# Kernel optimization log

Measured on AMD Instinct MI355X. Metric: run time of the kernel, lower is better.

## Reference

```python
import jax, jax.numpy as jnp
import numpy as np

N_NODES = 50000


def _sage_conv(x, src, dst, W_l, b_l, W_r):
    # mean aggregation of source-node features at destination nodes
    msg_sum = jax.ops.segment_sum(x[src], dst, num_segments=N_NODES)  # [N, d_in]
    deg = jax.ops.segment_sum(jnp.ones((src.shape[0],), x.dtype), dst,
                              num_segments=N_NODES)  # [N]
    mean = msg_sum / jnp.maximum(deg, 1.0)[:, None]
    # SAGEConv: lin_l(aggr) + lin_r(x); lin_l has bias, lin_r does not
    return mean @ W_l + b_l + x @ W_r


def setup_inputs() -> dict:
    key = jax.random.key(0)
    ks = jax.random.split(key, 8)
    d_in, d_hid, d_out = 128, 128, 64
    E = 800000
    s = lambda k, shp: jax.random.normal(k, shp, dtype=jnp.float32) * (1.0 / np.sqrt(shp[0]))
    return {
        "x": jax.random.normal(ks[0], (N_NODES, d_in), dtype=jnp.float32),
        "edge_index": jax.random.randint(ks[1], (2, E), 0, N_NODES, dtype=jnp.int64
                                         if jax.config.jax_enable_x64 else jnp.int32),
        "W_l1": s(ks[2], (d_in, d_hid)),
        "b_l1": jnp.zeros((d_hid,), jnp.float32),
        "W_r1": s(ks[3], (d_in, d_hid)),
        "W_l2": s(ks[4], (d_hid, d_out)),
        "b_l2": jnp.zeros((d_out,), jnp.float32),
        "W_r2": s(ks[5], (d_hid, d_out)),
    }


def reference(x, edge_index, W_l1, b_l1, W_r1, W_l2, b_l2, W_r2):
    src, dst = edge_index[0], edge_index[1]
    h = _sage_conv(x, src, dst, W_l1, b_l1, W_r1)
    h = jax.nn.relu(h)  # dropout is identity in eval mode
    h = _sage_conv(h, src, dst, W_l2, b_l2, W_r2)
    return h
```

## Files before the change

kernel.cpp:

```cpp
#include <hip/hip_runtime.h>
#include <hip/hip_bf16.h>

#define N_NODES 50000
#define M_TILES 3125
#define NBUCKET 196
#define CHUNK_A 3125
#define PASSB_CAP 12288
#define CONV_BLOCKS 6250

typedef __attribute__((ext_vector_type(8))) __bf16 bf16x8;
typedef __attribute__((ext_vector_type(4))) float f32x4;

#define OFF_OFF   0
#define EBUF_OFF  400384
#define GCUR_OFF  2000384
#define GBASE_OFF 2001408
#define CCNT_OFF  2002432
#define INV_OFF   3800576
#define XBF_OFF   4000768
#define AGG_OFF   16800768
#define HBF_OFF   29600768
#define PBF_OFF   42400768
#define WP1_OFF   48800768
#define WP2_OFF   48866304

__device__ __forceinline__ unsigned bfbits(float f) {
    unsigned u = __float_as_uint(f);
    return (u + 0x7fffu + ((u >> 16) & 1u)) & 0xffff0000u;
}
__device__ __forceinline__ unsigned short bf16r(float f) {
    return (unsigned short)(bfbits(f) >> 16);
}
__device__ __forceinline__ float blo(unsigned u) { return __uint_as_float(u << 16); }
__device__ __forceinline__ float bhi(unsigned u) { return __uint_as_float(u & 0xffff0000u); }

__global__ __launch_bounds__(256) void prep_kernel(const float4* __restrict__ x4,
                                                   uint2* __restrict__ xbf,
                                                   int* __restrict__ ccnt,
                                                   const float* __restrict__ Wl1,
                                                   const float* __restrict__ Wr1,
                                                   const float* __restrict__ Wl2,
                                                   const float* __restrict__ Wr2,
                                                   unsigned short* __restrict__ Wp1,
                                                   unsigned short* __restrict__ Wp2) {
    int bid = blockIdx.x;
    int t = threadIdx.x;
    if (bid < CONV_BLOCKS) {
        if (bid == 0 && t < NBUCKET) ccnt[t] = 0;
        int i = bid * 256 + t;
        float4 v = x4[i];
        uint2 o;
        o.x = (bfbits(v.x) >> 16) | bfbits(v.y);
        o.y = (bfbits(v.z) >> 16) | bfbits(v.w);
        xbf[i] = o;
    } else if (bid < CONV_BLOCKS + 128) {
        int idx = (bid - CONV_BLOCKS) * 256 + t;
        int k = idx >> 7, n = idx & 127;
        float v = (k < 128) ? Wl1[k * 128 + n] : Wr1[(k - 128) * 128 + n];
        Wp1[((k >> 5) << 12) + (n << 5) + (((k >> 3) & 3) << 3) + (k & 7)] = bf16r(v);
    } else {
        int idx = (bid - CONV_BLOCKS - 128) * 256 + t;
        int k = idx >> 7, n = idx & 127;
        float v = (n < 64) ? Wl2[k * 64 + n] : Wr2[k * 64 + (n - 64)];
        Wp2[((k >> 5) << 12) + (n << 5) + (((k >> 3) & 3) << 3) + (k & 7)] = bf16r(v);
    }
}

__global__ __launch_bounds__(256) void histC_kernel(const int* __restrict__ dst,
                                                    int* __restrict__ ccnt, int E) {
    __shared__ int lh[256];
    int t = threadIdx.x;
    lh[t] = 0;
    __syncthreads();
    int e0 = blockIdx.x * CHUNK_A;
    int e1 = min(e0 + CHUNK_A, E);
    for (int e = e0 + t; e < e1; e += 256) atomicAdd(&lh[dst[e] >> 8], 1);
    __syncthreads();
    if (lh[t]) atomicAdd(&ccnt[t], lh[t]);
}

__global__ __launch_bounds__(256) void scanG_kernel(const int* __restrict__ ccnt,
                                                    int* __restrict__ gbase,
                                                    int* __restrict__ gcur,
                                                    int* __restrict__ off, int E) {
    __shared__ int sm[256];
    int t = threadIdx.x;
    int v = (t < NBUCKET) ? ccnt[t] : 0;
    sm[t] = v;
    __syncthreads();
    for (int d = 1; d < 256; d <<= 1) {
        int u = (t >= d) ? sm[t - d] : 0;
        __syncthreads();
        sm[t] += u;
        __syncthreads();
    }
    int excl = sm[t] - v;
    if (t < NBUCKET) {
        gbase[t] = excl;
        gcur[t] = excl;
    }
    if (t == 0) {
        gbase[NBUCKET] = E;
        off[N_NODES] = E;
    }
}

__global__ __launch_bounds__(256) void passA_kernel(const int* __restrict__ src,
                                                    const int* __restrict__ dst,
                                                    int* __restrict__ gcur,
                                                    unsigned* __restrict__ pairs, int E) {
    __shared__ int bh[256];
    __shared__ int lcur[256];
    __shared__ int gb[256];
    __shared__ int sc[256];
    __shared__ unsigned lbuf[3328];
    int t = threadIdx.x;
    int e0 = blockIdx.x * CHUNK_A;
    int e1 = min(e0 + CHUNK_A, E);
    bh[t] = 0;
    lcur[t] = 0;
    __syncthreads();
    for (int e = e0 + t; e < e1; e += 256) atomicAdd(&bh[dst[e] >> 8], 1);
    __syncthreads();
    int v = bh[t];
    sc[t] = v;
    __syncthreads();
    for (int d = 1; d < 256; d <<= 1) {
        int u = (t >= d) ? sc[t - d] : 0;
        __syncthreads();
        sc[t] += u;
        __syncthreads();
    }
    int lbase = sc[t] - v;
    if (v > 0) gb[t] = atomicAdd(&gcur[t], v);
    bh[t] = lbase;
    __syncthreads();
    for (int e = e0 + t; e < e1; e += 256) {
        int s = src[e], d = dst[e];
        int b = d >> 8;
        int lpos = bh[b] + atomicAdd(&lcur[b], 1);
        lbuf[lpos] = (unsigned)s | ((unsigned)d << 16);
    }
    __syncthreads();
    int T = e1 - e0;
    for (int k = t; k < T; k += 256) {
        unsigned p = lbuf[k];
        int b = p >> 24;
        pairs[gb[b] + (k - bh[b])] = p;
    }
}

__global__ __launch_bounds__(256) void passB_kernel(const int* __restrict__ gbase,
                                                    const unsigned* __restrict__ pairs,
                                                    int* __restrict__ off,
                                                    float* __restrict__ invdeg,
                                                    unsigned short* __restrict__ ebuf16) {
    __shared__ int fh[256];
    __shared__ int sc[256];
    __shared__ int lcnt[256];
    __shared__ unsigned short lout[PASSB_CAP];
    int b = blockIdx.x;
    int t = threadIdx.x;
    int gb = gbase[b];
    int W = gbase[b + 1] - gb;
    fh[t] = 0;
    __syncthreads();
    for (int k = t; k < W; k += 256) atomicAdd(&fh[(pairs[gb + k] >> 16) & 255], 1);
    __syncthreads();
    int c = fh[t];
    sc[t] = c;
    __syncthreads();
    for (int d = 1; d < 256; d <<= 1) {
        int u = (t >= d) ? sc[t - d] : 0;
        __syncthreads();
        sc[t] += u;
        __syncthreads();
    }
    int excl = sc[t] - c;
    int dg = b * 256 + t;
    if (dg < N_NODES) {
        off[dg] = gb + excl;
        invdeg[dg] = 1.0f / fmaxf((float)c, 1.0f);
    }
    lcnt[t] = excl;
    __syncthreads();
    if (W <= PASSB_CAP) {
        for (int k = t; k < W; k += 256) {
            unsigned p = pairs[gb + k];
            int dl = (p >> 16) & 255;
            int pos = atomicAdd(&lcnt[dl], 1);
            lout[pos] = (unsigned short)(p & 0xffffu);
        }
        __syncthreads();
        for (int k = t; k < W; k += 256) ebuf16[gb + k] = lout[k];
    } else {
        for (int k = t; k < W; k += 256) {
            unsigned p = pairs[gb + k];
            int dl = (p >> 16) & 255;
            int pos = atomicAdd(&lcnt[dl], 1);
            ebuf16[gb + pos] = (unsigned short)(p & 0xffffu);
        }
    }
}

__global__ __launch_bounds__(64) void gather1_kernel(const int* __restrict__ off,
                                                     const unsigned short* __restrict__ ebuf,
                                                     const float* __restrict__ invdeg,
                                                     const uint4* __restrict__ xbf4,
                                                     uint4* __restrict__ aggbf4) {
    int d = blockIdx.x;
    int j = threadIdx.x;
    int g = j >> 4;
    int f = j & 15;
    int lo = off[d], hi = off[d + 1];
    float a[8] = {0.f, 0.f, 0.f, 0.f, 0.f, 0.f, 0.f, 0.f};
    int i = lo + g;
    for (; i + 4 < hi; i += 8) {
        int s0 = ebuf[i];
        int s1 = ebuf[i + 4];
        uint4 v0 = xbf4[(size_t)s0 * 16 + f];
        uint4 v1 = xbf4[(size_t)s1 * 16 + f];
        a[0] += blo(v0.x) + blo(v1.x); a[1] += bhi(v0.x) + bhi(v1.x);
        a[2] += blo(v0.y) + blo(v1.y); a[3] += bhi(v0.y) + bhi(v1.y);
        a[4] += blo(v0.z) + blo(v1.z); a[5] += bhi(v0.z) + bhi(v1.z);
        a[6] += blo(v0.w) + blo(v1.w); a[7] += bhi(v0.w) + bhi(v1.w);
    }
    if (i < hi) {
        uint4 v = xbf4[(size_t)ebuf[i] * 16 + f];
        a[0] += blo(v.x); a[1] += bhi(v.x);
        a[2] += blo(v.y); a[3] += bhi(v.y);
        a[4] += blo(v.z); a[5] += bhi(v.z);
        a[6] += blo(v.w); a[7] += bhi(v.w);
    }
#pragma unroll
    for (int q = 0; q < 8; ++q) {
        a[q] += __shfl_xor(a[q], 16, 64);
        a[q] += __shfl_xor(a[q], 32, 64);
    }
    if (g == 0) {
        float inv = invdeg[d];
        uint4 o;
        o.x = (bfbits(a[0] * inv) >> 16) | bfbits(a[1] * inv);
        o.y = (bfbits(a[2] * inv) >> 16) | bfbits(a[3] * inv);
        o.z = (bfbits(a[4] * inv) >> 16) | bfbits(a[5] * inv);
        o.w = (bfbits(a[6] * inv) >> 16) | bfbits(a[7] * inv);
        aggbf4[(size_t)d * 16 + f] = o;
    }
}

__global__ __launch_bounds__(256) void gemm1_kernel(const unsigned short* __restrict__ aggbf,
                                                    const unsigned short* __restrict__ xbf,
                                                    const unsigned short* __restrict__ Wp1,
                                                    const float* __restrict__ b1,
                                                    unsigned short* __restrict__ hbf) {
    int tile = blockIdx.x * 4 + (threadIdx.x >> 6);
    if (tile >= M_TILES) return;
    int lane = threadIdx.x & 63;
    int lo16 = lane & 15;
    int kg = lane >> 4;
    int m0 = tile * 16;

    f32x4 acc[8];
#pragma unroll
    for (int n = 0; n < 8; ++n) acc[n] = (f32x4){0.f, 0.f, 0.f, 0.f};

    int arow = m0 + lo16;
    const unsigned short* rowa = aggbf + (size_t)arow * 128;
    const unsigned short* rowx = xbf + (size_t)arow * 128;

#pragma unroll
    for (int ks = 0; ks < 8; ++ks) {
        const unsigned short* abase =
            (ks < 4 ? rowa + ks * 32 : rowx + (ks - 4) * 32) + kg * 8;
        bf16x8 a = *reinterpret_cast<const bf16x8*>(abase);
        const unsigned short* wbase = Wp1 + ks * 4096 + lo16 * 32 + kg * 8;
#pragma unroll
        for (int n = 0; n < 8; ++n) {
            bf16x8 b = *reinterpret_cast<const bf16x8*>(wbase + n * 512);
            acc[n] = __builtin_amdgcn_mfma_f32_16x16x32_bf16(a, b, acc[n], 0, 0, 0);
        }
    }

    int r0 = (lane >> 4) * 4;
#pragma unroll
    for (int n = 0; n < 8; ++n) {
        int col = n * 16 + lo16;
        float bv = b1[col];
#pragma unroll
        for (int r = 0; r < 4; ++r) {
            int row = m0 + r0 + r;
            float v = acc[n][r] + bv;
            hbf[(size_t)row * 128 + col] = bf16r(fmaxf(v, 0.0f));
        }
    }
}

__global__ __launch_bounds__(256) void gemm2_kernel(const unsigned short* __restrict__ hbf,
                                                    const unsigned short* __restrict__ Wp2,
                                                    const float* __restrict__ b2,
                                                    unsigned short* __restrict__ pbf,
                                                    float* __restrict__ out) {
    int tile = blockIdx.x * 4 + (threadIdx.x >> 6);
    if (tile >= M_TILES) return;
    int lane = threadIdx.x & 63;
    int lo16 = lane & 15;
    int kg = lane >> 4;
    int m0 = tile * 16;

    f32x4 acc[8];
#pragma unroll
    for (int n = 0; n < 8; ++n) acc[n] = (f32x4){0.f, 0.f, 0.f, 0.f};

    const unsigned short* rowh = hbf + (size_t)(m0 + lo16) * 128;

#pragma unroll
    for (int ks = 0; ks < 4; ++ks) {
        bf16x8 a = *reinterpret_cast<const bf16x8*>(rowh + ks * 32 + kg * 8);
        const unsigned short* wbase = Wp2 + ks * 4096 + lo16 * 32 + kg * 8;
#pragma unroll
        for (int n = 0; n < 8; ++n) {
            bf16x8 b = *reinterpret_cast<const bf16x8*>(wbase + n * 512);
            acc[n] = __builtin_amdgcn_mfma_f32_16x16x32_bf16(a, b, acc[n], 0, 0, 0);
        }
    }

    int r0 = (lane >> 4) * 4;
#pragma unroll
    for (int n = 0; n < 8; ++n) {
        int col = n * 16 + lo16;
        if (col < 64) {
#pragma unroll
            for (int r = 0; r < 4; ++r) {
                int row = m0 + r0 + r;
                pbf[(size_t)row * 64 + col] = bf16r(acc[n][r]);
            }
        } else {
            float bv = b2[col - 64];
#pragma unroll
            for (int r = 0; r < 4; ++r) {
                int row = m0 + r0 + r;
                out[(size_t)row * 64 + (col - 64)] = acc[n][r] + bv;
            }
        }
    }
}

__global__ __launch_bounds__(64) void gather2_kernel(const int* __restrict__ off,
                                                     const unsigned short* __restrict__ ebuf,
                                                     const float* __restrict__ invdeg,
                                                     const uint2* __restrict__ pbf2,
                                                     float4* __restrict__ out4) {
    int d = blockIdx.x;
    int j = threadIdx.x;
    int g = j >> 4;
    int f = j & 15;
    int lo = off[d], hi = off[d + 1];
    float a0 = 0.f, a1 = 0.f, a2 = 0.f, a3 = 0.f;
    int i = lo + g;
    for (; i + 4 < hi; i += 8) {
        int s0 = ebuf[i];
        int s1 = ebuf[i + 4];
        uint2 v0 = pbf2[(size_t)s0 * 16 + f];
        uint2 v1 = pbf2[(size_t)s1 * 16 + f];
        a0 += blo(v0.x) + blo(v1.x); a1 += bhi(v0.x) + bhi(v1.x);
        a2 += blo(v0.y) + blo(v1.y); a3 += bhi(v0.y) + bhi(v1.y);
    }
    if (i < hi) {
        uint2 v = pbf2[(size_t)ebuf[i] * 16 + f];
        a0 += blo(v.x); a1 += bhi(v.x);
        a2 += blo(v.y); a3 += bhi(v.y);
    }
    a0 += __shfl_xor(a0, 16, 64); a0 += __shfl_xor(a0, 32, 64);
    a1 += __shfl_xor(a1, 16, 64); a1 += __shfl_xor(a1, 32, 64);
    a2 += __shfl_xor(a2, 16, 64); a2 += __shfl_xor(a2, 32, 64);
    a3 += __shfl_xor(a3, 16, 64); a3 += __shfl_xor(a3, 32, 64);
    if (g == 0) {
        float inv = invdeg[d];
        float4* op = out4 + (size_t)d * 16 + f;
        float4 o = *op;
        o.x += a0 * inv;
        o.y += a1 * inv;
        o.z += a2 * inv;
        o.w += a3 * inv;
        *op = o;
    }
}

extern "C" void kernel_launch(void* const* d_in, const int* in_sizes, int n_in,
                              void* d_out, int out_size, void* d_ws, size_t ws_size,
                              hipStream_t stream) {
    const float* x   = (const float*)d_in[0];
    const int*   ei  = (const int*)d_in[1];
    const float* Wl1 = (const float*)d_in[2];
    const float* b1  = (const float*)d_in[3];
    const float* Wr1 = (const float*)d_in[4];
    const float* Wl2 = (const float*)d_in[5];
    const float* b2  = (const float*)d_in[6];
    const float* Wr2 = (const float*)d_in[7];
    float* out = (float*)d_out;

    const int E = in_sizes[1] / 2;
    const int* src = ei;
    const int* dst = ei + E;

    char* ws = (char*)d_ws;
    int*            off    = (int*)(ws + OFF_OFF);
    unsigned short* ebuf16 = (unsigned short*)(ws + EBUF_OFF);
    int*            gcur   = (int*)(ws + GCUR_OFF);
    int*            gbase  = (int*)(ws + GBASE_OFF);
    int*            ccnt   = (int*)(ws + CCNT_OFF);
    float*          invdeg = (float*)(ws + INV_OFF);
    unsigned*       xbf    = (unsigned*)(ws + XBF_OFF);
    unsigned*       aggbf  = (unsigned*)(ws + AGG_OFF);
    unsigned short* hbf    = (unsigned short*)(ws + HBF_OFF);
    unsigned*       pairs  = (unsigned*)(ws + HBF_OFF);
    unsigned short* pbf    = (unsigned short*)(ws + PBF_OFF);
    unsigned short* Wp1    = (unsigned short*)(ws + WP1_OFF);
    unsigned short* Wp2    = (unsigned short*)(ws + WP2_OFF);

    prep_kernel<<<CONV_BLOCKS + 192, 256, 0, stream>>>((const float4*)x, (uint2*)xbf, ccnt,
                                                       Wl1, Wr1, Wl2, Wr2, Wp1, Wp2);

    histC_kernel<<<(E + CHUNK_A - 1) / CHUNK_A, 256, 0, stream>>>(dst, ccnt, E);
    scanG_kernel<<<1, 256, 0, stream>>>(ccnt, gbase, gcur, off, E);
    passA_kernel<<<(E + CHUNK_A - 1) / CHUNK_A, 256, 0, stream>>>(src, dst, gcur, pairs, E);
    passB_kernel<<<NBUCKET, 256, 0, stream>>>(gbase, pairs, off, invdeg, ebuf16);

    gather1_kernel<<<N_NODES, 64, 0, stream>>>(off, ebuf16, invdeg, (const uint4*)xbf,
                                               (uint4*)aggbf);
    gemm1_kernel<<<(M_TILES + 3) / 4, 256, 0, stream>>>((const unsigned short*)aggbf,
                                                        (const unsigned short*)xbf, Wp1, b1, hbf);

    gemm2_kernel<<<(M_TILES + 3) / 4, 256, 0, stream>>>(hbf, Wp2, b2, pbf, out);
    gather2_kernel<<<N_NODES, 64, 0, stream>>>(off, ebuf16, invdeg, (const uint2*)pbf,
                                               (float4*)out);
}
```

Measured before the change: 132.4 us.

## Fuse two GEMMs through LDS, drop scan kernel, unroll gathers deeper

Fuses the layer-1 GEMM (with bias and ReLU) into the layer-2 GEMM: the hidden tile is staged in swizzled shared memory instead of being written to and reread from global memory. The separate single-block scan kernel is removed, and each passA/passB block recomputes the bucket prefix sum from the counts, with gcur zeroed in histC. The gather loops are unrolled to four edges per iteration to keep more loads in flight. This saves a kernel launch and the hidden-activation round trip, at the cost of redundant scans per block and more registers.

```diff
diff --git a/kernel.cpp b/kernel.cpp
--- a/kernel.cpp
+++ b/kernel.cpp
@@ -14,12 +14,11 @@
 #define OFF_OFF   0
 #define EBUF_OFF  400384
 #define GCUR_OFF  2000384
-#define GBASE_OFF 2001408
 #define CCNT_OFF  2002432
 #define INV_OFF   3800576
 #define XBF_OFF   4000768
 #define AGG_OFF   16800768
-#define HBF_OFF   29600768
+#define PAIRS_OFF 29600768
 #define PBF_OFF   42400768
 #define WP1_OFF   48800768
 #define WP2_OFF   48866304
@@ -67,9 +66,11 @@
 }
 
 __global__ __launch_bounds__(256) void histC_kernel(const int* __restrict__ dst,
-                                                    int* __restrict__ ccnt, int E) {
+                                                    int* __restrict__ ccnt,
+                                                    int* __restrict__ gcur, int E) {
     __shared__ int lh[256];
     int t = threadIdx.x;
+    if (blockIdx.x == 0 && t < NBUCKET) gcur[t] = 0;
     lh[t] = 0;
     __syncthreads();
     int e0 = blockIdx.x * CHUNK_A;
@@ -79,34 +80,9 @@
     if (lh[t]) atomicAdd(&ccnt[t], lh[t]);
 }
 
-__global__ __launch_bounds__(256) void scanG_kernel(const int* __restrict__ ccnt,
-                                                    int* __restrict__ gbase,
-                                                    int* __restrict__ gcur,
-                                                    int* __restrict__ off, int E) {
-    __shared__ int sm[256];
-    int t = threadIdx.x;
-    int v = (t < NBUCKET) ? ccnt[t] : 0;
-    sm[t] = v;
-    __syncthreads();
-    for (int d = 1; d < 256; d <<= 1) {
-        int u = (t >= d) ? sm[t - d] : 0;
-        __syncthreads();
-        sm[t] += u;
-        __syncthreads();
-    }
-    int excl = sm[t] - v;
-    if (t < NBUCKET) {
-        gbase[t] = excl;
-        gcur[t] = excl;
-    }
-    if (t == 0) {
-        gbase[NBUCKET] = E;
-        off[N_NODES] = E;
-    }
-}
-
 __global__ __launch_bounds__(256) void passA_kernel(const int* __restrict__ src,
                                                     const int* __restrict__ dst,
+                                                    const int* __restrict__ ccnt,
                                                     int* __restrict__ gcur,
                                                     unsigned* __restrict__ pairs, int E) {
     __shared__ int bh[256];
@@ -115,6 +91,16 @@
     __shared__ int sc[256];
     __shared__ unsigned lbuf[3328];
     int t = threadIdx.x;
+    int cc = (t < NBUCKET) ? ccnt[t] : 0;
+    sc[t] = cc;
+    __syncthreads();
+    for (int d = 1; d < 256; d <<= 1) {
+        int u = (t >= d) ? sc[t - d] : 0;
+        __syncthreads();
+        sc[t] += u;
+        __syncthreads();
+    }
+    int gbase_t = sc[t] - cc;
     int e0 = blockIdx.x * CHUNK_A;
     int e1 = min(e0 + CHUNK_A, E);
     bh[t] = 0;
@@ -132,7 +118,7 @@
         __syncthreads();
     }
     int lbase = sc[t] - v;
-    if (v > 0) gb[t] = atomicAdd(&gcur[t], v);
+    if (v > 0) gb[t] = gbase_t + atomicAdd(&gcur[t], v);
     bh[t] = lbase;
     __syncthreads();
     for (int e = e0 + t; e < e1; e += 256) {
@@ -150,21 +136,32 @@
     }
 }
 
-__global__ __launch_bounds__(256) void passB_kernel(const int* __restrict__ gbase,
+__global__ __launch_bounds__(256) void passB_kernel(const int* __restrict__ ccnt,
                                                     const unsigned* __restrict__ pairs,
                                                     int* __restrict__ off,
                                                     float* __restrict__ invdeg,
-                                                    unsigned short* __restrict__ ebuf16) {
+                                                    unsigned short* __restrict__ ebuf16,
+                                                    int E) {
+    __shared__ int sc[256];
     __shared__ int fh[256];
-    __shared__ int sc[256];
     __shared__ int lcnt[256];
+    __shared__ int sGb, sW;
     __shared__ unsigned short lout[PASSB_CAP];
     int b = blockIdx.x;
     int t = threadIdx.x;
-    int gb = gbase[b];
-    int W = gbase[b + 1] - gb;
+    int cc = (t < NBUCKET) ? ccnt[t] : 0;
+    sc[t] = cc;
+    __syncthreads();
+    for (int d = 1; d < 256; d <<= 1) {
+        int u = (t >= d) ? sc[t - d] : 0;
+        __syncthreads();
+        sc[t] += u;
+        __syncthreads();
+    }
+    if (t == b) { sGb = sc[t] - cc; sW = cc; }
     fh[t] = 0;
     __syncthreads();
+    int gb = sGb, W = sW;
     for (int k = t; k < W; k += 256) atomicAdd(&fh[(pairs[gb + k] >> 16) & 255], 1);
     __syncthreads();
     int c = fh[t];
@@ -182,6 +179,7 @@
         off[dg] = gb + excl;
         invdeg[dg] = 1.0f / fmaxf((float)c, 1.0f);
     }
+    if (b == NBUCKET - 1 && t == 0) off[N_NODES] = E;
     lcnt[t] = excl;
     __syncthreads();
     if (W <= PASSB_CAP) {
@@ -215,17 +213,22 @@
     int lo = off[d], hi = off[d + 1];
     float a[8] = {0.f, 0.f, 0.f, 0.f, 0.f, 0.f, 0.f, 0.f};
     int i = lo + g;
-    for (; i + 4 < hi; i += 8) {
-        int s0 = ebuf[i];
-        int s1 = ebuf[i + 4];
+    for (; i + 12 < hi; i += 16) {
+        int s0 = ebuf[i], s1 = ebuf[i + 4], s2 = ebuf[i + 8], s3 = ebuf[i + 12];
         uint4 v0 = xbf4[(size_t)s0 * 16 + f];
         uint4 v1 = xbf4[(size_t)s1 * 16 + f];
-        a[0] += blo(v0.x) + blo(v1.x); a[1] += bhi(v0.x) + bhi(v1.x);
-        a[2] += blo(v0.y) + blo(v1.y); a[3] += bhi(v0.y) + bhi(v1.y);
-        a[4] += blo(v0.z) + blo(v1.z); a[5] += bhi(v0.z) + bhi(v1.z);
-        a[6] += blo(v0.w) + blo(v1.w); a[7] += bhi(v0.w) + bhi(v1.w);
-    }
-    if (i < hi) {
+        uint4 v2 = xbf4[(size_t)s2 * 16 + f];
+        uint4 v3 = xbf4[(size_t)s3 * 16 + f];
+        a[0] += blo(v0.x) + blo(v1.x) + blo(v2.x) + blo(v3.x);
+        a[1] += bhi(v0.x) + bhi(v1.x) + bhi(v2.x) + bhi(v3.x);
+        a[2] += blo(v0.y) + blo(v1.y) + blo(v2.y) + blo(v3.y);
+        a[3] += bhi(v0.y) + bhi(v1.y) + bhi(v2.y) + bhi(v3.y);
+        a[4] += blo(v0.z) + blo(v1.z) + blo(v2.z) + blo(v3.z);
+        a[5] += bhi(v0.z) + bhi(v1.z) + bhi(v2.z) + bhi(v3.z);
+        a[6] += blo(v0.w) + blo(v1.w) + blo(v2.w) + blo(v3.w);
+        a[7] += bhi(v0.w) + bhi(v1.w) + bhi(v2.w) + bhi(v3.w);
+    }
+    for (; i < hi; i += 4) {
         uint4 v = xbf4[(size_t)ebuf[i] * 16 + f];
         a[0] += blo(v.x); a[1] += bhi(v.x);
         a[2] += blo(v.y); a[3] += bhi(v.y);
@@ -248,26 +251,30 @@
     }
 }
 
-__global__ __launch_bounds__(256) void gemm1_kernel(const unsigned short* __restrict__ aggbf,
+__global__ __launch_bounds__(256) void gemmF_kernel(const unsigned short* __restrict__ aggbf,
                                                     const unsigned short* __restrict__ xbf,
                                                     const unsigned short* __restrict__ Wp1,
                                                     const float* __restrict__ b1,
-                                                    unsigned short* __restrict__ hbf) {
-    int tile = blockIdx.x * 4 + (threadIdx.x >> 6);
-    if (tile >= M_TILES) return;
+                                                    const unsigned short* __restrict__ Wp2,
+                                                    const float* __restrict__ b2,
+                                                    unsigned short* __restrict__ pbf,
+                                                    float* __restrict__ out) {
+    __shared__ unsigned short hsm[4][2048];
+    int w = threadIdx.x >> 6;
+    int tile = blockIdx.x * 4 + w;
+    bool active = tile < M_TILES;
+    if (!active) tile = M_TILES - 1;
     int lane = threadIdx.x & 63;
     int lo16 = lane & 15;
     int kg = lane >> 4;
     int m0 = tile * 16;
+    int r0 = kg * 4;
 
     f32x4 acc[8];
 #pragma unroll
     for (int n = 0; n < 8; ++n) acc[n] = (f32x4){0.f, 0.f, 0.f, 0.f};
-
-    int arow = m0 + lo16;
-    const unsigned short* rowa = aggbf + (size_t)arow * 128;
-    const unsigned short* rowx = xbf + (size_t)arow * 128;
-
+    const unsigned short* rowa = aggbf + (size_t)(m0 + lo16) * 128;
+    const unsigned short* rowx = xbf + (size_t)(m0 + lo16) * 128;
 #pragma unroll
     for (int ks = 0; ks < 8; ++ks) {
         const unsigned short* abase =
@@ -281,50 +288,36 @@
         }
     }
 
-    int r0 = (lane >> 4) * 4;
+    unsigned short* hs = hsm[w];
 #pragma unroll
     for (int n = 0; n < 8; ++n) {
         int col = n * 16 + lo16;
         float bv = b1[col];
 #pragma unroll
         for (int r = 0; r < 4; ++r) {
-            int row = m0 + r0 + r;
-            float v = acc[n][r] + bv;
-            hbf[(size_t)row * 128 + col] = bf16r(fmaxf(v, 0.0f));
-        }
-    }
-}
-
-__global__ __launch_bounds__(256) void gemm2_kernel(const unsigned short* __restrict__ hbf,
-                                                    const unsigned short* __restrict__ Wp2,
-                                                    const float* __restrict__ b2,
-                                                    unsigned short* __restrict__ pbf,
-                                                    float* __restrict__ out) {
-    int tile = blockIdx.x * 4 + (threadIdx.x >> 6);
-    if (tile >= M_TILES) return;
-    int lane = threadIdx.x & 63;
-    int lo16 = lane & 15;
-    int kg = lane >> 4;
-    int m0 = tile * 16;
-
-    f32x4 acc[8];
-#pragma unroll
-    for (int n = 0; n < 8; ++n) acc[n] = (f32x4){0.f, 0.f, 0.f, 0.f};
-
-    const unsigned short* rowh = hbf + (size_t)(m0 + lo16) * 128;
-
+            int row = r0 + r;
+            float v = fmaxf(acc[n][r] + bv, 0.0f);
+            hs[row * 128 + (col ^ ((row & 7) << 3))] = bf16r(v);
+        }
+    }
+    __syncthreads();
+
+    f32x4 acc2[8];
+#pragma unroll
+    for (int n = 0; n < 8; ++n) acc2[n] = (f32x4){0.f, 0.f, 0.f, 0.f};
 #pragma unroll
     for (int ks = 0; ks < 4; ++ks) {
-        bf16x8 a = *reinterpret_cast<const bf16x8*>(rowh + ks * 32 + kg * 8);
+        int base0 = (ks * 32 + kg * 8) ^ ((lo16 & 7) << 3);
+        bf16x8 a2 = *reinterpret_cast<const bf16x8*>(&hs[lo16 * 128 + base0]);
         const unsigned short* wbase = Wp2 + ks * 4096 + lo16 * 32 + kg * 8;
 #pragma unroll
         for (int n = 0; n < 8; ++n) {
             bf16x8 b = *reinterpret_cast<const bf16x8*>(wbase + n * 512);
-            acc[n] = __builtin_amdgcn_mfma_f32_16x16x32_bf16(a, b, acc[n], 0, 0, 0);
-        }
-    }
-
-    int r0 = (lane >> 4) * 4;
+            acc2[n] = __builtin_amdgcn_mfma_f32_16x16x32_bf16(a2, b, acc2[n], 0, 0, 0);
+        }
+    }
+
+    if (!active) return;
 #pragma unroll
     for (int n = 0; n < 8; ++n) {
         int col = n * 16 + lo16;
@@ -332,14 +325,14 @@
 #pragma unroll
             for (int r = 0; r < 4; ++r) {
                 int row = m0 + r0 + r;
-                pbf[(size_t)row * 64 + col] = bf16r(acc[n][r]);
+                pbf[(size_t)row * 64 + col] = bf16r(acc2[n][r]);
             }
         } else {
             float bv = b2[col - 64];
 #pragma unroll
             for (int r = 0; r < 4; ++r) {
                 int row = m0 + r0 + r;
-                out[(size_t)row * 64 + (col - 64)] = acc[n][r] + bv;
+                out[(size_t)row * 64 + (col - 64)] = acc2[n][r] + bv;
             }
         }
     }
@@ -357,15 +350,18 @@
     int lo = off[d], hi = off[d + 1];
     float a0 = 0.f, a1 = 0.f, a2 = 0.f, a3 = 0.f;
     int i = lo + g;
-    for (; i + 4 < hi; i += 8) {
-        int s0 = ebuf[i];
-        int s1 = ebuf[i + 4];
+    for (; i + 12 < hi; i += 16) {
+        int s0 = ebuf[i], s1 = ebuf[i + 4], s2 = ebuf[i + 8], s3 = ebuf[i + 12];
         uint2 v0 = pbf2[(size_t)s0 * 16 + f];
         uint2 v1 = pbf2[(size_t)s1 * 16 + f];
-        a0 += blo(v0.x) + blo(v1.x); a1 += bhi(v0.x) + bhi(v1.x);
-        a2 += blo(v0.y) + blo(v1.y); a3 += bhi(v0.y) + bhi(v1.y);
-    }
-    if (i < hi) {
+        uint2 v2 = pbf2[(size_t)s2 * 16 + f];
+        uint2 v3 = pbf2[(size_t)s3 * 16 + f];
+        a0 += blo(v0.x) + blo(v1.x) + blo(v2.x) + blo(v3.x);
+        a1 += bhi(v0.x) + bhi(v1.x) + bhi(v2.x) + bhi(v3.x);
+        a2 += blo(v0.y) + blo(v1.y) + blo(v2.y) + blo(v3.y);
+        a3 += bhi(v0.y) + bhi(v1.y) + bhi(v2.y) + bhi(v3.y);
+    }
+    for (; i < hi; i += 4) {
         uint2 v = pbf2[(size_t)ebuf[i] * 16 + f];
         a0 += blo(v.x); a1 += bhi(v.x);
         a2 += blo(v.y); a3 += bhi(v.y);
@@ -407,13 +403,11 @@
     int*            off    = (int*)(ws + OFF_OFF);
     unsigned short* ebuf16 = (unsigned short*)(ws + EBUF_OFF);
     int*            gcur   = (int*)(ws + GCUR_OFF);
-    int*            gbase  = (int*)(ws + GBASE_OFF);
     int*            ccnt   = (int*)(ws + CCNT_OFF);
     float*          invdeg = (float*)(ws + INV_OFF);
     unsigned*       xbf    = (unsigned*)(ws + XBF_OFF);
     unsigned*       aggbf  = (unsigned*)(ws + AGG_OFF);
-    unsigned short* hbf    = (unsigned short*)(ws + HBF_OFF);
-    unsigned*       pairs  = (unsigned*)(ws + HBF_OFF);
+    unsigned*       pairs  = (unsigned*)(ws + PAIRS_OFF);
     unsigned short* pbf    = (unsigned short*)(ws + PBF_OFF);
     unsigned short* Wp1    = (unsigned short*)(ws + WP1_OFF);
     unsigned short* Wp2    = (unsigned short*)(ws + WP2_OFF);
@@ -421,17 +415,18 @@
     prep_kernel<<<CONV_BLOCKS + 192, 256, 0, stream>>>((const float4*)x, (uint2*)xbf, ccnt,
                                                        Wl1, Wr1, Wl2, Wr2, Wp1, Wp2);
 
-    histC_kernel<<<(E + CHUNK_A - 1) / CHUNK_A, 256, 0, stream>>>(dst, ccnt, E);
-    scanG_kernel<<<1, 256, 0, stream>>>(ccnt, gbase, gcur, off, E);
-    passA_kernel<<<(E + CHUNK_A - 1) / CHUNK_A, 256, 0, stream>>>(src, dst, gcur, pairs, E);
-    passB_kernel<<<NBUCKET, 256, 0, stream>>>(gbase, pairs, off, invdeg, ebuf16);
+    histC_kernel<<<(E + CHUNK_A - 1) / CHUNK_A, 256, 0, stream>>>(dst, ccnt, gcur, E);
+    passA_kernel<<<(E + CHUNK_A - 1) / CHUNK_A, 256, 0, stream>>>(src, dst, ccnt, gcur,
+                                                                  pairs, E);
+    passB_kernel<<<NBUCKET, 256, 0, stream>>>(ccnt, pairs, off, invdeg, ebuf16, E);
 
     gather1_kernel<<<N_NODES, 64, 0, stream>>>(off, ebuf16, invdeg, (const uint4*)xbf,
                                                (uint4*)aggbf);
-    gemm1_kernel<<<(M_TILES + 3) / 4, 256, 0, stream>>>((const unsigned short*)aggbf,
-                                                        (const unsigned short*)xbf, Wp1, b1, hbf);
-
-    gemm2_kernel<<<(M_TILES + 3) / 4, 256, 0, stream>>>(hbf, Wp2, b2, pbf, out);
+
+    gemmF_kernel<<<(M_TILES + 3) / 4, 256, 0, stream>>>((const unsigned short*)aggbf,
+                                                        (const unsigned short*)xbf,
+                                                        Wp1, b1, Wp2, b2, pbf, out);
+
     gather2_kernel<<<N_NODES, 64, 0, stream>>>(off, ebuf16, invdeg, (const uint2*)pbf,
                                                (float4*)out);
 }
```

Result: faster. 126.7 us (-4.3%).
